# Kernel optimization log

Measured on AMD Instinct MI355X. Metric: run time of the kernel, lower is better.

Reference implementation:

```python
import jax, jax.numpy as jnp
import numpy as np

B, S, D, H = 4, 1024, 1024, 16
DH = D // H  # head dim = 64
PAD = -1e7   # padding_num in source
EPS = 1e-3   # keras LayerNormalization default epsilon


def setup_inputs() -> dict:
    key = jax.random.key(0)
    ks = jax.random.split(key, 8)
    return {
        "queries": jax.random.normal(ks[0], (B, S, D), jnp.float32),
        "keys": jax.random.normal(ks[1], (B, S, D), jnp.float32),
        "values": jax.random.normal(ks[2], (B, S, D), jnp.float32),
        "query_masks": jax.random.randint(ks[3], (B, S), 0, 2, jnp.int32),
        "key_masks": jax.random.randint(ks[4], (B, S), 0, 2, jnp.int32),
        "Wq": jax.random.normal(ks[5], (D, D), jnp.float32) * (D ** -0.5),
        "Wk": jax.random.normal(ks[6], (D, D), jnp.float32) * (D ** -0.5),
        "Wv": jax.random.normal(ks[7], (D, D), jnp.float32) * (D ** -0.5),
        "gamma": jnp.ones((D,), jnp.float32),
        "beta": jnp.zeros((D,), jnp.float32),
    }


def reference(queries, keys, values, query_masks, key_masks, Wq, Wk, Wv, gamma, beta):
    # QKV projections (no bias)
    Q = queries @ Wq  # [B,S,D]
    K = keys @ Wk
    V = values @ Wv
    # split heads: tf.split(axis=2)+concat(axis=0) == head-major layout [H,B,S,DH]
    Qh = Q.reshape(B, S, H, DH).transpose(2, 0, 1, 3)
    Kh = K.reshape(B, S, H, DH).transpose(2, 0, 1, 3)
    Vh = V.reshape(B, S, H, DH).transpose(2, 0, 1, 3)
    # scaled scores; note source scales by head_dim ** 0.5 (d_k of split K)
    scores = jnp.einsum("hbqd,hbkd->hbqk", Qh, Kh) / (DH ** 0.5)
    # additive key mask: positions where key_mask==0 get large negative
    scores = jnp.where(key_masks[None, :, None, :] == 0, PAD, scores)
    attn = jax.nn.softmax(scores, axis=-1)
    # multiplicative query mask AFTER softmax (as in source)
    attn = attn * query_masks[None, :, :, None].astype(jnp.float32)
    out = jnp.einsum("hbqk,hbkd->hbqd", attn, Vh)  # [H,B,S,DH]
    # merge heads back: concat over feature axis in head order
    out = out.transpose(1, 2, 0, 3).reshape(B, S, D)
    # residual + LayerNorm
    res = queries + out
    mean = jnp.mean(res, axis=-1, keepdims=True)
    var = jnp.mean(jnp.square(res - mean), axis=-1, keepdims=True)
    return gamma * (res - mean) * jax.lax.rsqrt(var + EPS) + beta
```

## Files before the change

kernel.cpp:

```cpp
#include <hip/hip_runtime.h>

#define BB   4
#define SS   1024
#define DD   1024
#define HH   16
#define DHH  64
#define LN_EPS  (1e-3f)

typedef unsigned short u16;
typedef __attribute__((ext_vector_type(8))) short bf16x8;
typedef __attribute__((ext_vector_type(4))) float f32x4;

__device__ __forceinline__ u16 f2bf(float f) {
    union { float f; unsigned int u; } v; v.f = f;
    return (u16)((v.u + 0x7FFFu + ((v.u >> 16) & 1u)) >> 16);
}

__device__ __forceinline__ unsigned int cvt_pk_bf16(float lo, float hi) {
    unsigned int r;
    asm("v_cvt_pk_bf16_f32 %0, %1, %2" : "=v"(r) : "v"(lo), "v"(hi));
    return r;
}

__device__ __forceinline__ void cp16(void* lds, const void* g) {
    __builtin_amdgcn_global_load_lds(
        (const __attribute__((address_space(1))) unsigned int*)g,
        (__attribute__((address_space(3))) unsigned int*)lds, 16, 0, 0);
}

__global__ __launch_bounds__(256) void prep(const float* __restrict__ q,
                                            const float* __restrict__ k,
                                            const float* __restrict__ v,
                                            const float* __restrict__ Wq,
                                            const float* __restrict__ Wk,
                                            const float* __restrict__ Wv,
                                            u16* __restrict__ Abf,
                                            u16* __restrict__ WtA) {
    __shared__ float Ts[64][65];
    const int z = blockIdx.z;
    const int tid = threadIdx.x;
    if (z < 3) {
        const float* src = (z == 0) ? q : (z == 1) ? k : v;
        u16* dst = Abf + (size_t)z * ((size_t)BB * SS * DD);
        const int N8 = BB * SS * DD / 8;
        for (int i = blockIdx.x * 256 + tid; i < N8; i += 256 * 256) {
            const float4 f0 = ((const float4*)src)[i * 2];
            const float4 f1 = ((const float4*)src)[i * 2 + 1];
            union { u16 u[8]; uint4 o; } t;
            t.u[0] = f2bf(f0.x); t.u[1] = f2bf(f0.y);
            t.u[2] = f2bf(f0.z); t.u[3] = f2bf(f0.w);
            t.u[4] = f2bf(f1.x); t.u[5] = f2bf(f1.y);
            t.u[6] = f2bf(f1.z); t.u[7] = f2bf(f1.w);
            ((uint4*)dst)[i] = t.o;
        }
    } else {
        const float* W = (z == 3) ? Wq : (z == 4) ? Wk : Wv;
        u16* Wt = WtA + (size_t)(z - 3) * DD * DD;
        const int k0 = (blockIdx.x >> 4) * 64, n0 = (blockIdx.x & 15) * 64;
        #pragma unroll
        for (int it = 0; it < 4; ++it) {
            const int idx = tid + it * 256;
            const int r = idx >> 4, c4 = (idx & 15) * 4;
            const float4 vv = *(const float4*)&W[(size_t)(k0 + r) * DD + n0 + c4];
            Ts[r][c4 + 0] = vv.x; Ts[r][c4 + 1] = vv.y;
            Ts[r][c4 + 2] = vv.z; Ts[r][c4 + 3] = vv.w;
        }
        __syncthreads();
        const int n = tid >> 2, kc = (tid & 3) * 16;
        #pragma unroll
        for (int p = 0; p < 8; ++p) {
            const unsigned int lo = f2bf(Ts[kc + p * 2 + 0][n]);
            const unsigned int hi = f2bf(Ts[kc + p * 2 + 1][n]);
            *(unsigned int*)&Wt[(size_t)(n0 + n) * DD + k0 + kc + p * 2] = lo | (hi << 16);
        }
    }
}

__global__ __launch_bounds__(256) void gemm_fused(const u16* __restrict__ Abf,
                                                  const u16* __restrict__ WtA,
                                                  u16* __restrict__ Qbf,
                                                  u16* __restrict__ Kbf,
                                                  u16* __restrict__ Vtb) {
    __shared__ u16 As[2][128 * 64];
    __shared__ u16 Bs[2][128 * 64];

    const int bid = blockIdx.x;
    const int swz = (bid & 7) * 96 + (bid >> 3);
    const int z   = swz >> 8;
    const int rem = swz & 255;
    const int m0  = (rem >> 3) * 128;
    const int n0  = (rem & 7) * 128;

    const u16* A  = Abf + (size_t)z * ((size_t)BB * SS * DD);
    const u16* Bm = WtA + (size_t)z * (DD * DD);

    const int tid  = threadIdx.x;
    const int wave = tid >> 6, lane = tid & 63;
    const int ln = lane & 15, quad = lane >> 4;
    const int mw = (wave & 1) * 64, nw = (wave >> 1) * 64;

    const u16* srcA[4];
    const u16* srcB[4];
    #pragma unroll
    for (int w = 0; w < 4; ++w) {
        const int l = w * 256 + tid;
        const int r = l >> 3, cs = l & 7;
        const int c = cs ^ (r & 7);
        srcA[w] = A  + (size_t)(m0 + r) * DD + c * 8;
        srcB[w] = Bm + (size_t)(n0 + r) * DD + c * 8;
    }

    auto stage = [&](int T) {
        const int cb = T & 1;
        const int koff = T * 64;
        #pragma unroll
        for (int w = 0; w < 4; ++w)
            cp16(&As[cb][(w * 256 + wave * 64) * 8], srcA[w] + koff);
        #pragma unroll
        for (int w = 0; w < 4; ++w)
            cp16(&Bs[cb][(w * 256 + wave * 64) * 8], srcB[w] + koff);
    };

    f32x4 acc[4][4] = {};

    stage(0);
    #pragma unroll
    for (int t = 0; t < 16; ++t) {
        const int cb = t & 1;
        if (t < 15) stage(t + 1);
        if (t < 15) asm volatile("s_waitcnt vmcnt(8)" ::: "memory");
        else        asm volatile("s_waitcnt vmcnt(0)" ::: "memory");
        __builtin_amdgcn_s_barrier();

        #pragma unroll
        for (int kk = 0; kk < 2; ++kk) {
            bf16x8 af[4], bfv[4];
            #pragma unroll
            for (int i = 0; i < 4; ++i) {
                const int r = mw + i * 16 + ln;
                af[i] = *(const bf16x8*)&As[cb][((r << 3) + ((kk * 4 + quad) ^ (r & 7))) << 3];
            }
            #pragma unroll
            for (int j = 0; j < 4; ++j) {
                const int r = nw + j * 16 + ln;
                bfv[j] = *(const bf16x8*)&Bs[cb][((r << 3) + ((kk * 4 + quad) ^ (r & 7))) << 3];
            }
            __builtin_amdgcn_s_setprio(1);
            #pragma unroll
            for (int i = 0; i < 4; ++i)
                #pragma unroll
                for (int j = 0; j < 4; ++j)
                    acc[i][j] = __builtin_amdgcn_mfma_f32_16x16x32_bf16(af[i], bfv[j], acc[i][j], 0, 0, 0);
            __builtin_amdgcn_s_setprio(0);
        }
        __builtin_amdgcn_s_barrier();
    }

    if (z < 2) {
        u16* C = (z == 0) ? Qbf : Kbf;
        const float scale = (z == 0) ? 0.18033688f : 1.0f;
        #pragma unroll
        for (int i = 0; i < 4; ++i) {
            const int mbase = m0 + mw + i * 16 + quad * 4;
            const int bb = mbase >> 10, sb = mbase & 1023;
            #pragma unroll
            for (int j = 0; j < 4; ++j) {
                const int n = n0 + nw + j * 16 + ln;
                const int hh = n >> 6, dh = n & 63;
                #pragma unroll
                for (int r = 0; r < 4; ++r)
                    C[(((size_t)bb * HH + hh) * SS + sb + r) * DHH + dh] =
                        f2bf(acc[i][j][r] * scale);
            }
        }
    } else {
        #pragma unroll
        for (int i = 0; i < 4; ++i) {
            const int mbase = m0 + mw + i * 16 + quad * 4;
            const int bb = mbase >> 10, sb = mbase & 1023;
            #pragma unroll
            for (int j = 0; j < 4; ++j) {
                const int n = n0 + nw + j * 16 + ln;
                const int hh = n >> 6, dh = n & 63;
                uint2 pk;
                pk.x = cvt_pk_bf16(acc[i][j][0], acc[i][j][1]);
                pk.y = cvt_pk_bf16(acc[i][j][2], acc[i][j][3]);
                *(uint2*)&Vtb[(((size_t)bb * HH + hh) * DHH + dh) * SS + sb] = pk;
            }
        }
    }
}

__global__ __launch_bounds__(512) void attn_mfma(const u16* __restrict__ Qg,
                                                 const u16* __restrict__ Kg,
                                                 const u16* __restrict__ Vtg,
                                                 const int* __restrict__ qmask,
                                                 const int* __restrict__ kmask,
                                                 float* __restrict__ O) {
    __shared__ u16 Ps[128 * 68];
    __shared__ u16 Ks[2][64 * 64];
    __shared__ u16 Vs[2][64 * 64];
    __shared__ float kmLds[SS];

    const int bid  = blockIdx.x;
    const int xcd  = bid & 7;
    const int rest = bid >> 3;
    const int bh   = (rest & 7) * 8 + xcd;
    const int qt   = rest >> 3;
    const int b    = bh >> 4, h = bh & 15;
    const int q0   = qt * 128;
    const int tid  = threadIdx.x;
    const int wave = tid >> 6, lane = tid & 63;
    const int ln = lane & 15, quad = lane >> 4;
    const size_t bhs = (size_t)b * HH + h;

    const int sr = tid >> 3, scsrc = (tid & 7) ^ ((tid >> 3) & 7);
    const u16* kSrc = &Kg[(bhs * SS + sr) * DHH + scsrc * 8];
    const u16* vSrc = &Vtg[(bhs * DHH + sr) * SS + scsrc * 8];
    auto stageKV = [&](int t) {
        const int cb = t & 1;
        cp16(&Ks[cb][wave * 512], kSrc + (size_t)t * 64 * DHH);
        cp16(&Vs[cb][wave * 512], vSrc + t * 64);
    };

    const u16* qrow = &Qg[(bhs * SS + q0 + wave * 16 + ln) * DHH];
    const bf16x8 qf0 = *(const bf16x8*)&qrow[quad * 8];
    const bf16x8 qf1 = *(const bf16x8*)&qrow[32 + quad * 8];
    asm volatile("" ::: "memory");
    if (wave < 4)
        cp16(&kmLds[wave * 256], &kmask[b * SS + (wave * 64 + lane) * 4]);
    stageKV(0);
    stageKV(1);
    asm volatile("s_waitcnt vmcnt(2)" ::: "memory");
    __builtin_amdgcn_s_barrier();

    {
        const int2 iv = *(const int2*)&kmLds[tid * 2];
        float2 fv; fv.x = (float)iv.x; fv.y = (float)iv.y;
        *(float2*)&kmLds[tid * 2] = fv;
    }
    asm volatile("s_waitcnt lgkmcnt(0)" ::: "memory");
    __builtin_amdgcn_s_barrier();

    int off[4][2];
    #pragma unroll
    for (int nt = 0; nt < 4; ++nt) {
        const int r = nt * 16 + ln;
        off[nt][0] = ((r << 3) + ((0 + quad) ^ (r & 7))) << 3;
        off[nt][1] = ((r << 3) + ((4 + quad) ^ (r & 7))) << 3;
    }

    f32x4 o[4] = {};
    float lsum = 0.f;
    const f32x4 zero = {0.f, 0.f, 0.f, 0.f};
    const int prow = (wave * 16 + ln) * 68;

    #pragma unroll 2
    for (int kt = 0; kt < SS / 64; ++kt) {
        const int cb = kt & 1;
        const u16* Kc = Ks[cb];
        const u16* Vc = Vs[cb];

        #pragma unroll
        for (int nt = 0; nt < 4; ++nt) {
            const bf16x8 k0f = *(const bf16x8*)&Kc[off[nt][0]];
            const bf16x8 k1f = *(const bf16x8*)&Kc[off[nt][1]];
            f32x4 sacc = __builtin_amdgcn_mfma_f32_16x16x32_bf16(k0f, qf0, zero, 0, 0, 0);
            sacc = __builtin_amdgcn_mfma_f32_16x16x32_bf16(k1f, qf1, sacc, 0, 0, 0);
            const float4 fm = *(const float4*)&kmLds[kt * 64 + nt * 16 + quad * 4];
            const float p0 = fm.x * __builtin_amdgcn_exp2f(sacc[0]);
            const float p1 = fm.y * __builtin_amdgcn_exp2f(sacc[1]);
            const float p2 = fm.z * __builtin_amdgcn_exp2f(sacc[2]);
            const float p3 = fm.w * __builtin_amdgcn_exp2f(sacc[3]);
            lsum += (p0 + p1) + (p2 + p3);
            uint2 pk;
            pk.x = cvt_pk_bf16(p0, p1);
            pk.y = cvt_pk_bf16(p2, p3);
            *(uint2*)&Ps[prow + nt * 16 + quad * 4] = pk;
        }

        __builtin_amdgcn_s_setprio(1);
        #pragma unroll
        for (int kk2 = 0; kk2 < 2; ++kk2) {
            const bf16x8 pf = *(const bf16x8*)&Ps[prow + kk2 * 32 + quad * 8];
            #pragma unroll
            for (int nt2 = 0; nt2 < 4; ++nt2) {
                const bf16x8 vf = *(const bf16x8*)&Vc[off[nt2][kk2]];
                o[nt2] = __builtin_amdgcn_mfma_f32_16x16x32_bf16(pf, vf, o[nt2], 0, 0, 0);
            }
        }
        __builtin_amdgcn_s_setprio(0);

        if (kt == SS / 64 - 1) break;
        __builtin_amdgcn_s_barrier();
        if (kt + 2 < SS / 64) {
            stageKV(kt + 2);
            asm volatile("s_waitcnt vmcnt(2)" ::: "memory");
        } else {
            asm volatile("s_waitcnt vmcnt(0)" ::: "memory");
        }
        __builtin_amdgcn_s_barrier();
    }

    lsum += __shfl_xor(lsum, 16);
    lsum += __shfl_xor(lsum, 32);
    #pragma unroll
    for (int r = 0; r < 4; ++r) {
        const int qloc = quad * 4 + r;
        const float l = __shfl(lsum, qloc);
        const int q = q0 + wave * 16 + qloc;
        const float scale = (float)qmask[b * SS + q] / l;
        #pragma unroll
        for (int nt2 = 0; nt2 < 4; ++nt2)
            O[((size_t)b * SS + q) * DD + h * DHH + nt2 * 16 + ln] = o[nt2][r] * scale;
    }
}

__global__ __launch_bounds__(256) void ln_kernel(const float* __restrict__ Qin,
                                                 const float* __restrict__ attn,
                                                 const float* __restrict__ gamma,
                                                 const float* __restrict__ beta,
                                                 float* __restrict__ out) {
    const int row = blockIdx.x;
    const int tid = threadIdx.x;
    const int wid = tid >> 6, lane = tid & 63;
    __shared__ float sred[4];

    const float4 qv = ((const float4*)Qin)[(size_t)row * 256 + tid];
    const float4 av = ((const float4*)attn)[(size_t)row * 256 + tid];
    float4 v;
    v.x = qv.x + av.x; v.y = qv.y + av.y;
    v.z = qv.z + av.z; v.w = qv.w + av.w;

    float sum = v.x + v.y + v.z + v.w;
    #pragma unroll
    for (int off = 32; off; off >>= 1) sum += __shfl_down(sum, off);
    if (lane == 0) sred[wid] = sum;
    __syncthreads();
    const float mean = (sred[0] + sred[1] + sred[2] + sred[3]) * (1.0f / DD);
    __syncthreads();

    const float dx = v.x - mean, dy = v.y - mean, dz = v.z - mean, dw = v.w - mean;
    float vs = dx * dx + dy * dy + dz * dz + dw * dw;
    #pragma unroll
    for (int off = 32; off; off >>= 1) vs += __shfl_down(vs, off);
    if (lane == 0) sred[wid] = vs;
    __syncthreads();
    const float var = (sred[0] + sred[1] + sred[2] + sred[3]) * (1.0f / DD);
    const float inv = rsqrtf(var + LN_EPS);

    const float4 g = ((const float4*)gamma)[tid];
    const float4 bt = ((const float4*)beta)[tid];
    float4 ov;
    ov.x = g.x * dx * inv + bt.x; ov.y = g.y * dy * inv + bt.y;
    ov.z = g.z * dz * inv + bt.z; ov.w = g.w * dw * inv + bt.w;
    ((float4*)out)[(size_t)row * 256 + tid] = ov;
}

extern "C" void kernel_launch(void* const* d_in, const int* in_sizes, int n_in,
                              void* d_out, int out_size, void* d_ws, size_t ws_size,
                              hipStream_t stream) {
    const float* queries = (const float*)d_in[0];
    const float* keys    = (const float*)d_in[1];
    const float* values  = (const float*)d_in[2];
    const int*   qmask   = (const int*)d_in[3];
    const int*   kmask   = (const int*)d_in[4];
    const float* Wq      = (const float*)d_in[5];
    const float* Wk      = (const float*)d_in[6];
    const float* Wv      = (const float*)d_in[7];
    const float* gamma   = (const float*)d_in[8];
    const float* beta    = (const float*)d_in[9];
    float* out = (float*)d_out;

    const size_t NTOK = (size_t)BB * SS;
    u16* Abf = (u16*)d_ws;
    float* Ob = (float*)d_ws;
    u16* Qbf = Abf + 3 * NTOK * DD;
    u16* Kbf = Qbf + NTOK * DD;
    u16* Vtb = Kbf + NTOK * DD;
    u16* WtA = Vtb + NTOK * DD;

    prep<<<dim3(256, 1, 6), 256, 0, stream>>>(queries, keys, values, Wq, Wk, Wv, Abf, WtA);

    gemm_fused<<<768, 256, 0, stream>>>(Abf, WtA, Qbf, Kbf, Vtb);

    attn_mfma<<<BB * HH * (SS / 128), 512, 0, stream>>>(Qbf, Kbf, Vtb, qmask, kmask, Ob);

    ln_kernel<<<BB * SS, 256, 0, stream>>>(queries, Ob, gamma, beta, out);
}
```

Baseline: 185.2 us.

## Single-buffer QKV GEMM LDS tiles to raise occupancy

Replaces the double-buffered LDS staging in the fused QKV projection GEMM with a single buffer guarded by two __syncthreads per k-step. It also drops the precomputed per-thread source pointer arrays and the full unroll of the k loop, and sets launch bounds to allow 3 blocks per CU. Halving LDS and trimming registers aims to raise occupancy so other blocks hide load latency. The cost is that copy/compute overlap inside a block is lost, since every tile load now waits fully before any MFMA runs.

```diff
diff --git a/kernel.cpp b/kernel.cpp
--- a/kernel.cpp
+++ b/kernel.cpp
@@ -76,13 +76,13 @@
     }
 }
 
-__global__ __launch_bounds__(256) void gemm_fused(const u16* __restrict__ Abf,
-                                                  const u16* __restrict__ WtA,
-                                                  u16* __restrict__ Qbf,
-                                                  u16* __restrict__ Kbf,
-                                                  u16* __restrict__ Vtb) {
-    __shared__ u16 As[2][128 * 64];
-    __shared__ u16 Bs[2][128 * 64];
+__global__ __launch_bounds__(256, 3) void gemm_fused(const u16* __restrict__ Abf,
+                                                     const u16* __restrict__ WtA,
+                                                     u16* __restrict__ Qbf,
+                                                     u16* __restrict__ Kbf,
+                                                     u16* __restrict__ Vtb) {
+    __shared__ u16 As[128 * 64];
+    __shared__ u16 Bs[128 * 64];
 
     const int bid = blockIdx.x;
     const int swz = (bid & 7) * 96 + (bid >> 3);
@@ -99,38 +99,22 @@
     const int ln = lane & 15, quad = lane >> 4;
     const int mw = (wave & 1) * 64, nw = (wave >> 1) * 64;
 
-    const u16* srcA[4];
-    const u16* srcB[4];
-    #pragma unroll
-    for (int w = 0; w < 4; ++w) {
-        const int l = w * 256 + tid;
-        const int r = l >> 3, cs = l & 7;
-        const int c = cs ^ (r & 7);
-        srcA[w] = A  + (size_t)(m0 + r) * DD + c * 8;
-        srcB[w] = Bm + (size_t)(n0 + r) * DD + c * 8;
-    }
-
-    auto stage = [&](int T) {
-        const int cb = T & 1;
-        const int koff = T * 64;
-        #pragma unroll
-        for (int w = 0; w < 4; ++w)
-            cp16(&As[cb][(w * 256 + wave * 64) * 8], srcA[w] + koff);
-        #pragma unroll
-        for (int w = 0; w < 4; ++w)
-            cp16(&Bs[cb][(w * 256 + wave * 64) * 8], srcB[w] + koff);
-    };
+    const int r0 = tid >> 3;
+    const int c0 = (tid & 7) ^ (r0 & 7);
+    const u16* srcA0 = A  + (size_t)(m0 + r0) * DD + c0 * 8;
+    const u16* srcB0 = Bm + (size_t)(n0 + r0) * DD + c0 * 8;
 
     f32x4 acc[4][4] = {};
 
-    stage(0);
-    #pragma unroll
     for (int t = 0; t < 16; ++t) {
-        const int cb = t & 1;
-        if (t < 15) stage(t + 1);
-        if (t < 15) asm volatile("s_waitcnt vmcnt(8)" ::: "memory");
-        else        asm volatile("s_waitcnt vmcnt(0)" ::: "memory");
-        __builtin_amdgcn_s_barrier();
+        const int koff = t * 64;
+        __syncthreads();
+        #pragma unroll
+        for (int w = 0; w < 4; ++w) {
+            cp16(&As[(w * 256 + wave * 64) * 8], srcA0 + (size_t)w * 32 * DD + koff);
+            cp16(&Bs[(w * 256 + wave * 64) * 8], srcB0 + (size_t)w * 32 * DD + koff);
+        }
+        __syncthreads();
 
         #pragma unroll
         for (int kk = 0; kk < 2; ++kk) {
@@ -138,12 +122,12 @@
             #pragma unroll
             for (int i = 0; i < 4; ++i) {
                 const int r = mw + i * 16 + ln;
-                af[i] = *(const bf16x8*)&As[cb][((r << 3) + ((kk * 4 + quad) ^ (r & 7))) << 3];
+                af[i] = *(const bf16x8*)&As[((r << 3) + ((kk * 4 + quad) ^ (r & 7))) << 3];
             }
             #pragma unroll
             for (int j = 0; j < 4; ++j) {
                 const int r = nw + j * 16 + ln;
-                bfv[j] = *(const bf16x8*)&Bs[cb][((r << 3) + ((kk * 4 + quad) ^ (r & 7))) << 3];
+                bfv[j] = *(const bf16x8*)&Bs[((r << 3) + ((kk * 4 + quad) ^ (r & 7))) << 3];
             }
             __builtin_amdgcn_s_setprio(1);
             #pragma unroll
@@ -153,7 +137,6 @@
                     acc[i][j] = __builtin_amdgcn_mfma_f32_16x16x32_bf16(af[i], bfv[j], acc[i][j], 0, 0, 0);
             __builtin_amdgcn_s_setprio(0);
         }
-        __builtin_amdgcn_s_barrier();
     }
 
     if (z < 2) {
```

Result: faster. 179.1 us (-3.3%).
